# Performance work log

Hardware: AMD Instinct MI355X
Metric: run time of the kernel (lower is better)

The kernel has to match this reference:

```python
import jax, jax.numpy as jnp
import numpy as np

IN_DIM = 256
OUT_DIM = 256


def setup_inputs() -> dict:
    key = jax.random.key(0)
    k1, k2, k3, k4 = jax.random.split(key, 4)
    B, N = 8, 2048
    X = jax.random.normal(k1, (B, N, IN_DIM), dtype=jnp.float32)
    adj = jax.random.uniform(k2, (B, N, N), dtype=jnp.float32)
    # nn.Linear(input_dim, output_dim): W is [out, in], bias [out]
    bound = 1.0 / np.sqrt(IN_DIM)
    W = jax.random.uniform(k3, (OUT_DIM, IN_DIM), minval=-bound, maxval=bound, dtype=jnp.float32)
    b = jax.random.uniform(k4, (OUT_DIM,), minval=-bound, maxval=bound, dtype=jnp.float32)
    return {"X": X, "adj": adj, "W": W, "b": b}


def reference(X, adj, W, b):
    N = adj.shape[-1]
    # adj_hat = adj + I
    adj_hat = adj + jnp.eye(N, dtype=adj.dtype)
    # D^{-1/2} A_hat D^{-1/2}: diag matmuls are just row/col scaling
    d = jnp.sum(adj_hat, axis=-1) ** -0.5  # [B, N]
    adj_norm = d[..., :, None] * adj_hat * d[..., None, :]
    # aggregate then linear + relu
    H = jnp.matmul(adj_norm, X)  # [B, N, F_in]
    out = jnp.einsum('bnf,of->bno', H, W) + b
    return jax.nn.relu(out)
```

## Files before the change

### kernel.cpp

```cpp
#include <hip/hip_runtime.h>
#include <stdint.h>

typedef __attribute__((ext_vector_type(8))) short bf16x8;
typedef __attribute__((ext_vector_type(4))) float f32x4;
typedef unsigned short u16;

constexpr int NN = 2048, NF = 256;

__device__ inline u16 f2bf(float f) {
  uint32_t u = __builtin_bit_cast(uint32_t, f);
  uint32_t r = (u + 0x7FFFu + ((u >> 16) & 1u)) >> 16;
  return (u16)r;
}

__device__ inline void gload_lds16(const void* g, void* l) {
  __builtin_amdgcn_global_load_lds(
      (const __attribute__((address_space(1))) uint32_t*)g,
      (__attribute__((address_space(3))) uint32_t*)l,
      16, 0, 0);
}

__global__ __launch_bounds__(256) void k_rowsum(const float* __restrict__ adj,
                                                float* __restrict__ d) {
  int row = blockIdx.x;
  const float4* p = (const float4*)(adj + (size_t)row * NN);
  float s = 0.f;
#pragma unroll
  for (int c = 0; c < 2; ++c) {
    float4 v = p[threadIdx.x + 256 * c];
    s += v.x + v.y + v.z + v.w;
  }
#pragma unroll
  for (int off = 32; off > 0; off >>= 1) s += __shfl_down(s, off, 64);
  __shared__ float red[4];
  int lane = threadIdx.x & 63, w = threadIdx.x >> 6;
  if (lane == 0) red[w] = s;
  __syncthreads();
  if (threadIdx.x == 0) {
    float t = red[0] + red[1] + red[2] + red[3] + 1.0f;
    d[row] = 1.0f / sqrtf(t);
  }
}

__global__ __launch_bounds__(256) void k_wconv(const float* __restrict__ W,
                                               u16* __restrict__ Wb) {
  int i = blockIdx.x * 256 + threadIdx.x;
  float4 v = ((const float4*)W)[i];
  ushort4 o;
  o.x = f2bf(v.x); o.y = f2bf(v.y); o.z = f2bf(v.z); o.w = f2bf(v.w);
  *(ushort4*)(Wb + (size_t)i * 4) = o;
}

__global__ __launch_bounds__(256) void k_xprep(const float* __restrict__ X,
                                               const float* __restrict__ d,
                                               u16* __restrict__ XpT) {
  int jt = blockIdx.x, ft = blockIdx.y, b = blockIdx.z;
  int j0 = jt * 64, f0 = ft * 64;
  __shared__ u16 T[64][66];
  int t = threadIdx.x;
#pragma unroll
  for (int s = 0; s < 4; ++s) {
    int q = s * 256 + t;
    int r = q >> 4, c4 = q & 15;
    int j = j0 + r;
    float dv = d[b * NN + j];
    float4 v = *(const float4*)(X + ((size_t)(b * NN + j)) * NF + f0 + c4 * 4);
    T[r][c4 * 4 + 0] = f2bf(v.x * dv);
    T[r][c4 * 4 + 1] = f2bf(v.y * dv);
    T[r][c4 * 4 + 2] = f2bf(v.z * dv);
    T[r][c4 * 4 + 3] = f2bf(v.w * dv);
  }
  __syncthreads();
#pragma unroll
  for (int s = 0; s < 4; ++s) {
    int q = s * 256 + t;
    int fr = q >> 4, c4 = q & 15;
    int f = f0 + fr;
    int swz = (f >> 1) & 3;
    int joff = (c4 * 4) ^ (swz << 3);
    ushort4 o;
    o.x = T[c4 * 4 + 0][fr]; o.y = T[c4 * 4 + 1][fr];
    o.z = T[c4 * 4 + 2][fr]; o.w = T[c4 * 4 + 3][fr];
    *(ushort4*)(XpT + ((size_t)(b * NF + f)) * NN + j0 + joff) = o;
  }
}

__global__ __launch_bounds__(256, 2) void k_fused(
    const float* __restrict__ adj, const u16* __restrict__ XpT,
    const float* __restrict__ X, const float* __restrict__ dsc,
    const u16* __restrict__ Wb, const float* __restrict__ bias,
    float* __restrict__ out) {
  int flat = blockIdx.x;
  int b = flat & 7, mt = flat >> 3;
  int i0 = mt * 32;

  __shared__ __align__(16) char smem[36864];
  u16* Hs = (u16*)smem;

  int t = threadIdx.x;
  int lane = t & 63, w = t >> 6;
  int l15 = lane & 15, l4 = lane >> 4;
  int wc = w;

  const float* adjb = adj + ((size_t)b * NN + i0) * NN;
  const u16* XpTb = XpT + (size_t)b * NF * NN;

  int ar = t >> 3, ac4 = t & 7;
  const float* a_row = adjb + (size_t)ar * NN + ac4 * 4;
  int a_chunk = (ac4 >> 1) ^ ((ar >> 1) & 3);
  int a_wr_off = ar * 64 + a_chunk * 16 + (ac4 & 1) * 8;

  f32x4 acc[2][4] = {};

  {
    float4 araw = *(const float4*)(a_row);
#pragma unroll
    for (int c = 0; c < 4; ++c) {
      int q = c * 256 + t;
      gload_lds16(XpTb + (size_t)(q >> 2) * NN + (q & 3) * 8,
                  smem + 4096 + (size_t)(c * 256 + w * 64) * 16);
    }
    ushort4 o;
    o.x = f2bf(araw.x); o.y = f2bf(araw.y);
    o.z = f2bf(araw.z); o.w = f2bf(araw.w);
    *(ushort4*)(smem + a_wr_off) = o;
  }
  __syncthreads();

  for (int k = 0; k < 64; ++k) {
    char* Ac = smem + ((k & 1) << 11);
    char* An = smem + (((k & 1) ^ 1) << 11);
    char* Bc = smem + 4096 + ((k & 1) << 14);
    char* Bn = smem + 4096 + (((k & 1) ^ 1) << 14);

    bf16x8 af[2], bfr[4];
#pragma unroll
    for (int mi = 0; mi < 2; ++mi) {
      int r = mi * 16 + l15;
      af[mi] = *(const bf16x8*)(Ac + r * 64 + ((l4 ^ ((r >> 1) & 3)) << 4));
    }
#pragma unroll
    for (int ni = 0; ni < 4; ++ni) {
      int n = wc * 64 + ni * 16 + l15;
      bfr[ni] = *(const bf16x8*)(Bc + n * 64 + ((l4 ^ ((n >> 1) & 3)) << 4));
    }
    __builtin_amdgcn_sched_barrier(0);

    float4 araw2;
    if (k < 63) {
      araw2 = *(const float4*)(a_row + (k + 1) * 32);
      int k2 = (k + 1) * 32;
#pragma unroll
      for (int c = 0; c < 4; ++c) {
        int q = c * 256 + t;
        gload_lds16(XpTb + (size_t)(q >> 2) * NN + k2 + (q & 3) * 8,
                    Bn + (size_t)(c * 256 + w * 64) * 16);
      }
    }
    __builtin_amdgcn_sched_barrier(0);

    __builtin_amdgcn_s_setprio(1);
#pragma unroll
    for (int mi = 0; mi < 2; ++mi)
#pragma unroll
      for (int ni = 0; ni < 4; ++ni)
        acc[mi][ni] = __builtin_amdgcn_mfma_f32_16x16x32_bf16(af[mi], bfr[ni],
                                                              acc[mi][ni], 0, 0, 0);
    __builtin_amdgcn_s_setprio(0);
    __builtin_amdgcn_sched_barrier(0);

    if (k < 63) {
      ushort4 o;
      o.x = f2bf(araw2.x); o.y = f2bf(araw2.y);
      o.z = f2bf(araw2.z); o.w = f2bf(araw2.w);
      *(ushort4*)(An + a_wr_off) = o;
    }
    __syncthreads();
  }

  const float* db = dsc + b * NN;
  const float* Xb = X + ((size_t)b * NN + i0) * NF;
#pragma unroll
  for (int mi = 0; mi < 2; ++mi) {
#pragma unroll
    for (int qq = 0; qq < 4; ++qq) {
      int il = mi * 16 + l4 * 4 + qq;
      float dv = db[i0 + il];
      float dv2 = dv * dv;
#pragma unroll
      for (int ni = 0; ni < 4; ++ni) {
        int f = wc * 64 + ni * 16 + l15;
        float hv = dv * acc[mi][ni][qq] + dv2 * Xb[(size_t)il * NF + f];
        Hs[il * 264 + f] = f2bf(hv);
      }
    }
  }
  __syncthreads();

  f32x4 acc2[2][4] = {};
#pragma unroll
  for (int kk = 0; kk < 256; kk += 32) {
    bf16x8 a2[2], b2[4];
#pragma unroll
    for (int mi = 0; mi < 2; ++mi) {
      int r = mi * 16 + l15;
      a2[mi] = *(const bf16x8*)&Hs[r * 264 + kk + l4 * 8];
    }
#pragma unroll
    for (int ni = 0; ni < 4; ++ni) {
      int o = wc * 64 + ni * 16 + l15;
      b2[ni] = *(const bf16x8*)&Wb[(size_t)o * 256 + kk + l4 * 8];
    }
#pragma unroll
    for (int mi = 0; mi < 2; ++mi)
#pragma unroll
      for (int ni = 0; ni < 4; ++ni)
        acc2[mi][ni] = __builtin_amdgcn_mfma_f32_16x16x32_bf16(a2[mi], b2[ni],
                                                               acc2[mi][ni], 0, 0, 0);
  }

  float* outb = out + ((size_t)b * NN + i0) * NF;
#pragma unroll
  for (int mi = 0; mi < 2; ++mi) {
#pragma unroll
    for (int qq = 0; qq < 4; ++qq) {
      int il = mi * 16 + l4 * 4 + qq;
#pragma unroll
      for (int ni = 0; ni < 4; ++ni) {
        int o = wc * 64 + ni * 16 + l15;
        float v = acc2[mi][ni][qq] + bias[o];
        outb[(size_t)il * NF + o] = fmaxf(v, 0.f);
      }
    }
  }
}

extern "C" void kernel_launch(void* const* d_in, const int* in_sizes, int n_in,
                              void* d_out, int out_size, void* d_ws, size_t ws_size,
                              hipStream_t stream) {
  const float* X    = (const float*)d_in[0];
  const float* adj  = (const float*)d_in[1];
  const float* W    = (const float*)d_in[2];
  const float* bias = (const float*)d_in[3];
  float* out = (float*)d_out;

  char* ws = (char*)d_ws;
  float* dsc = (float*)(ws);
  u16*   Wb  = (u16*)(ws + 65536);
  u16*   XpT = (u16*)(ws + 262144);

  k_rowsum<<<dim3(16384), dim3(256), 0, stream>>>(adj, dsc);
  k_wconv<<<dim3(64), dim3(256), 0, stream>>>(W, Wb);
  k_xprep<<<dim3(32, 4, 8), dim3(256), 0, stream>>>(X, dsc, XpT);
  k_fused<<<dim3(512), dim3(256), 0, stream>>>(adj, XpT, X, dsc, Wb, bias, out);
}
```

Baseline: 89.83 us.

## Pre-convert adjacency to bf16 in rowsum and stream it via async LDS loads

```diff
diff --git a/kernel.cpp b/kernel.cpp
--- a/kernel.cpp
+++ b/kernel.cpp
@@ -11,6 +11,10 @@
   uint32_t u = __builtin_bit_cast(uint32_t, f);
   uint32_t r = (u + 0x7FFFu + ((u >> 16) & 1u)) >> 16;
   return (u16)r;
+}
+__device__ inline float bf2f(u16 h) {
+  uint32_t u = ((uint32_t)h) << 16;
+  return __builtin_bit_cast(float, u);
 }
 
 __device__ inline void gload_lds16(const void* g, void* l) {
@@ -21,14 +25,30 @@
 }
 
 __global__ __launch_bounds__(256) void k_rowsum(const float* __restrict__ adj,
-                                                float* __restrict__ d) {
+                                                u16* __restrict__ adjb,
+                                                float* __restrict__ d,
+                                                const float* __restrict__ W,
+                                                u16* __restrict__ Wb) {
+  if (blockIdx.x >= 16384) {
+    int i = (blockIdx.x - 16384) * 256 + threadIdx.x;
+    float4 v = ((const float4*)W)[i];
+    ushort4 o;
+    o.x = f2bf(v.x); o.y = f2bf(v.y); o.z = f2bf(v.z); o.w = f2bf(v.w);
+    *(ushort4*)(Wb + (size_t)i * 4) = o;
+    return;
+  }
   int row = blockIdx.x;
   const float4* p = (const float4*)(adj + (size_t)row * NN);
+  u16* ob = adjb + (size_t)row * NN;
   float s = 0.f;
 #pragma unroll
   for (int c = 0; c < 2; ++c) {
-    float4 v = p[threadIdx.x + 256 * c];
+    int idx = threadIdx.x + 256 * c;
+    float4 v = p[idx];
     s += v.x + v.y + v.z + v.w;
+    ushort4 o;
+    o.x = f2bf(v.x); o.y = f2bf(v.y); o.z = f2bf(v.z); o.w = f2bf(v.w);
+    *(ushort4*)(ob + (size_t)idx * 4) = o;
   }
 #pragma unroll
   for (int off = 32; off > 0; off >>= 1) s += __shfl_down(s, off, 64);
@@ -40,15 +60,6 @@
     float t = red[0] + red[1] + red[2] + red[3] + 1.0f;
     d[row] = 1.0f / sqrtf(t);
   }
-}
-
-__global__ __launch_bounds__(256) void k_wconv(const float* __restrict__ W,
-                                               u16* __restrict__ Wb) {
-  int i = blockIdx.x * 256 + threadIdx.x;
-  float4 v = ((const float4*)W)[i];
-  ushort4 o;
-  o.x = f2bf(v.x); o.y = f2bf(v.y); o.z = f2bf(v.z); o.w = f2bf(v.w);
-  *(ushort4*)(Wb + (size_t)i * 4) = o;
 }
 
 __global__ __launch_bounds__(256) void k_xprep(const float* __restrict__ X,
@@ -86,10 +97,9 @@
 }
 
 __global__ __launch_bounds__(256, 2) void k_fused(
-    const float* __restrict__ adj, const u16* __restrict__ XpT,
-    const float* __restrict__ X, const float* __restrict__ dsc,
-    const u16* __restrict__ Wb, const float* __restrict__ bias,
-    float* __restrict__ out) {
+    const u16* __restrict__ adjb, const u16* __restrict__ XpT,
+    const float* __restrict__ dsc, const u16* __restrict__ Wb,
+    const float* __restrict__ bias, float* __restrict__ out) {
   int flat = blockIdx.x;
   int b = flat & 7, mt = flat >> 3;
   int i0 = mt * 32;
@@ -102,28 +112,21 @@
   int l15 = lane & 15, l4 = lane >> 4;
   int wc = w;
 
-  const float* adjb = adj + ((size_t)b * NN + i0) * NN;
+  const u16* adjbb = adjb + ((size_t)b * NN + i0) * NN;
   const u16* XpTb = XpT + (size_t)b * NF * NN;
 
-  int ar = t >> 3, ac4 = t & 7;
-  const float* a_row = adjb + (size_t)ar * NN + ac4 * 4;
-  int a_chunk = (ac4 >> 1) ^ ((ar >> 1) & 3);
-  int a_wr_off = ar * 64 + a_chunk * 16 + (ac4 & 1) * 8;
+  int rl = (w << 3) + ((lane & 31) >> 2);
+  int asrc_off = ((lane & 3) ^ ((rl >> 1) & 3)) * 8;
+  const u16* a_src = adjbb + (size_t)rl * NN + asrc_off;
 
   f32x4 acc[2][4] = {};
 
-  {
-    float4 araw = *(const float4*)(a_row);
-#pragma unroll
-    for (int c = 0; c < 4; ++c) {
-      int q = c * 256 + t;
-      gload_lds16(XpTb + (size_t)(q >> 2) * NN + (q & 3) * 8,
-                  smem + 4096 + (size_t)(c * 256 + w * 64) * 16);
-    }
-    ushort4 o;
-    o.x = f2bf(araw.x); o.y = f2bf(araw.y);
-    o.z = f2bf(araw.z); o.w = f2bf(araw.w);
-    *(ushort4*)(smem + a_wr_off) = o;
+  if (lane < 32) gload_lds16(a_src, smem + (w << 9));
+#pragma unroll
+  for (int c = 0; c < 4; ++c) {
+    int q = c * 256 + t;
+    gload_lds16(XpTb + (size_t)(q >> 2) * NN + (q & 3) * 8,
+                smem + 4096 + (size_t)(c * 256 + w * 64) * 16);
   }
   __syncthreads();
 
@@ -146,10 +149,9 @@
     }
     __builtin_amdgcn_sched_barrier(0);
 
-    float4 araw2;
     if (k < 63) {
-      araw2 = *(const float4*)(a_row + (k + 1) * 32);
       int k2 = (k + 1) * 32;
+      if (lane < 32) gload_lds16(a_src + k2, An + (w << 9));
 #pragma unroll
       for (int c = 0; c < 4; ++c) {
         int q = c * 256 + t;
@@ -168,29 +170,24 @@
                                                               acc[mi][ni], 0, 0, 0);
     __builtin_amdgcn_s_setprio(0);
     __builtin_amdgcn_sched_barrier(0);
-
-    if (k < 63) {
-      ushort4 o;
-      o.x = f2bf(araw2.x); o.y = f2bf(araw2.y);
-      o.z = f2bf(araw2.z); o.w = f2bf(araw2.w);
-      *(ushort4*)(An + a_wr_off) = o;
-    }
     __syncthreads();
   }
 
   const float* db = dsc + b * NN;
-  const float* Xb = X + ((size_t)b * NN + i0) * NF;
 #pragma unroll
   for (int mi = 0; mi < 2; ++mi) {
 #pragma unroll
-    for (int qq = 0; qq < 4; ++qq) {
-      int il = mi * 16 + l4 * 4 + qq;
-      float dv = db[i0 + il];
-      float dv2 = dv * dv;
-#pragma unroll
-      for (int ni = 0; ni < 4; ++ni) {
-        int f = wc * 64 + ni * 16 + l15;
-        float hv = dv * acc[mi][ni][qq] + dv2 * Xb[(size_t)il * NF + f];
+    for (int ni = 0; ni < 4; ++ni) {
+      int f = wc * 64 + ni * 16 + l15;
+      int swz8 = ((f >> 1) & 3) << 3;
+      ushort4 xv = *(const ushort4*)(XpTb + (size_t)f * NN + i0 +
+                                     ((mi * 16 + l4 * 4) ^ swz8));
+#pragma unroll
+      for (int qq = 0; qq < 4; ++qq) {
+        int il = mi * 16 + l4 * 4 + qq;
+        float dv = db[i0 + il];
+        float xpv = bf2f(((const u16*)&xv)[qq]);
+        float hv = dv * (acc[mi][ni][qq] + xpv);
         Hs[il * 264 + f] = f2bf(hv);
       }
     }
@@ -245,12 +242,12 @@
   float* out = (float*)d_out;
 
   char* ws = (char*)d_ws;
-  float* dsc = (float*)(ws);
-  u16*   Wb  = (u16*)(ws + 65536);
-  u16*   XpT = (u16*)(ws + 262144);
-
-  k_rowsum<<<dim3(16384), dim3(256), 0, stream>>>(adj, dsc);
-  k_wconv<<<dim3(64), dim3(256), 0, stream>>>(W, Wb);
+  float* dsc  = (float*)(ws);
+  u16*   Wb   = (u16*)(ws + 65536);
+  u16*   XpT  = (u16*)(ws + 262144);
+  u16*   adjb = (u16*)(ws + 262144 + 8388608);
+
+  k_rowsum<<<dim3(16448), dim3(256), 0, stream>>>(adj, adjb, dsc, W, Wb);
   k_xprep<<<dim3(32, 4, 8), dim3(256), 0, stream>>>(X, dsc, XpT);
-  k_fused<<<dim3(512), dim3(256), 0, stream>>>(adj, XpT, X, dsc, Wb, bias, out);
-}
+  k_fused<<<dim3(512), dim3(256), 0, stream>>>(adjb, XpT, dsc, Wb, bias, out);
+}
```

New measurement: 85.73 us. 4.6% less time.
